# Kernel tuning notes

Measured on AMD Instinct MI355X. Metric: run time of the kernel, lower is better.

Reference implementation:

```python
import jax, jax.numpy as jnp
import numpy as np

V, D, B, NEGS = 100000, 128, 131072, 15
P_DROP = 0.1


def setup_inputs() -> dict:
    key = jax.random.key(0)
    k_t, k_c, k_n, k_m, k_wt = jax.random.split(key, 5)
    target = jax.random.randint(k_t, (B,), 0, V, dtype=jnp.int32)
    context = jax.random.randint(k_c, (B,), 0, V, dtype=jnp.int32)
    # multinomial over uniform noise_dist == uniform randint, with replacement
    neg_idx = jax.random.randint(k_n, (B, NEGS), 0, V, dtype=jnp.int32)
    # inverted dropout mask, p=0.1 (F.dropout default training=True)
    keep = jax.random.uniform(k_m, (B, D)) >= P_DROP
    dropout_mask = keep.astype(jnp.float32) / (1.0 - P_DROP)
    # embeddings_target init: uniform(-0.5/D, 0.5/D); embeddings_context init is zeros
    # in the original, but use small randn so the loss/grads are non-degenerate.
    r = 0.5 / D
    W_target = jax.random.uniform(k_wt, (V, D), minval=-r, maxval=r, dtype=jnp.float32)
    W_context = jax.random.normal(jax.random.fold_in(key, 7), (V, D), dtype=jnp.float32) * r
    return {"target": target, "context": context, "neg_idx": neg_idx,
            "dropout_mask": dropout_mask, "W_target": W_target, "W_context": W_context}


def reference(target, context, neg_idx, dropout_mask, W_target, W_context):
    emb_input = W_target[target] * dropout_mask          # [B, D]
    emb_context = W_context[context]                     # [B, D]
    score = jnp.sum(emb_input * emb_context, axis=1)     # [B]
    pos_loss = jax.nn.log_sigmoid(-score)                # [B]  (matches logsigmoid(-score))
    emb_neg = W_context[neg_idx]                         # [B, NEGS, D]
    neg_score = jnp.einsum('bnd,bd->bn', -emb_neg, emb_input)  # bmm(neg(emb_neg), emb_input)
    noise_loss = jnp.sum(jax.nn.log_sigmoid(neg_score), axis=1)  # [B]
    return -jnp.mean(pos_loss + noise_loss)
```

## Files before the change

kernel.cpp:

```cpp
#include <hip/hip_runtime.h>


#define V_SZ  100000
#define B_TOT 131072
#define DDIM  128
#define NNEG  15
#define NROWS 16
#define SCALE     512.0f
#define INV_SCALE (1.0f / 512.0f)

typedef float floatx2 __attribute__((ext_vector_type(2)));

__device__ __forceinline__ float log_sigmoid_fast(float x) {
    return fminf(x, 0.0f) - __logf(1.0f + __expf(-fabsf(x)));
}

__global__ __launch_bounds__(256) void convert_wc_fp8(
    const float* __restrict__ Wc, uint2* __restrict__ Wc8)
{
    const size_t t = (size_t)blockIdx.x * 256 + threadIdx.x;
    const float4* src = (const float4*)Wc;
    float4 a = src[2 * t];
    float4 b = src[2 * t + 1];
    int lo = 0, hi = 0;
    lo = __builtin_amdgcn_cvt_pk_fp8_f32(a.x * SCALE, a.y * SCALE, lo, false);
    lo = __builtin_amdgcn_cvt_pk_fp8_f32(a.z * SCALE, a.w * SCALE, lo, true);
    hi = __builtin_amdgcn_cvt_pk_fp8_f32(b.x * SCALE, b.y * SCALE, hi, false);
    hi = __builtin_amdgcn_cvt_pk_fp8_f32(b.z * SCALE, b.w * SCALE, hi, true);
    Wc8[t] = make_uint2((unsigned)lo, (unsigned)hi);
}

#define BPB   32
#define NBLK  (B_TOT / BPB)
#define RB    8

__global__ __launch_bounds__(256, 4) void cbow_main_fp8(
    const int* __restrict__ target, const int* __restrict__ context,
    const int* __restrict__ neg_idx, const float* __restrict__ dmask,
    const float* __restrict__ Wt, const unsigned* __restrict__ Wc8,
    float* __restrict__ block_sums)
{
    const int tid  = threadIdx.x;
    const int wave = tid >> 6;
    const int lane = tid & 63;
    const int grp  = lane >> 3;
    const int sub  = lane & 7;
    const int b = blockIdx.x * BPB + wave * 8 + grp;

    const int tgt = target[b];
    const float4* trow = (const float4*)(Wt + (size_t)tgt * DDIM) + 4 * sub;
    const float4* mrow = (const float4*)(dmask + (size_t)b * DDIM) + 4 * sub;
    float e[16];
#pragma unroll
    for (int k = 0; k < 4; ++k) {
        float4 w = trow[k];
        float4 m = mrow[k];
        e[4 * k + 0] = w.x * m.x * INV_SCALE;
        e[4 * k + 1] = w.y * m.y * INV_SCALE;
        e[4 * k + 2] = w.z * m.z * INV_SCALE;
        e[4 * k + 3] = w.w * m.w * INV_SCALE;
    }

    int ridx[NROWS];
    ridx[0] = context[b];
#pragma unroll
    for (int n = 0; n < NNEG; ++n)
        ridx[n + 1] = neg_idx[(size_t)b * NNEG + n];

    float acc = 0.0f;
    for (int rb = 0; rb < NROWS; rb += RB) {
        uint4 c[RB];
#pragma unroll
        for (int j = 0; j < RB; ++j)
            c[j] = ((const uint4*)(Wc8 + (size_t)ridx[rb + j] * (DDIM / 4)))[sub];
#pragma unroll
        for (int j = 0; j < RB; ++j) {
            floatx2 f0 = __builtin_amdgcn_cvt_pk_f32_fp8(c[j].x, false);
            floatx2 f1 = __builtin_amdgcn_cvt_pk_f32_fp8(c[j].x, true);
            floatx2 f2 = __builtin_amdgcn_cvt_pk_f32_fp8(c[j].y, false);
            floatx2 f3 = __builtin_amdgcn_cvt_pk_f32_fp8(c[j].y, true);
            floatx2 f4 = __builtin_amdgcn_cvt_pk_f32_fp8(c[j].z, false);
            floatx2 f5 = __builtin_amdgcn_cvt_pk_f32_fp8(c[j].z, true);
            floatx2 f6 = __builtin_amdgcn_cvt_pk_f32_fp8(c[j].w, false);
            floatx2 f7 = __builtin_amdgcn_cvt_pk_f32_fp8(c[j].w, true);
            float p = f0.x * e[0]  + f0.y * e[1]
                    + f1.x * e[2]  + f1.y * e[3]
                    + f2.x * e[4]  + f2.y * e[5]
                    + f3.x * e[6]  + f3.y * e[7]
                    + f4.x * e[8]  + f4.y * e[9]
                    + f5.x * e[10] + f5.y * e[11]
                    + f6.x * e[12] + f6.y * e[13]
                    + f7.x * e[14] + f7.y * e[15];
            p += __shfl_xor(p, 1);
            p += __shfl_xor(p, 2);
            p += __shfl_xor(p, 4);
            acc += log_sigmoid_fast(-p);
        }
    }

    if (sub != 0) acc = 0.0f;
    acc += __shfl_xor(acc, 8);
    acc += __shfl_xor(acc, 16);
    acc += __shfl_xor(acc, 32);

    __shared__ float wsum[4];
    if (lane == 0) wsum[wave] = acc;
    __syncthreads();
    if (tid == 0)
        block_sums[blockIdx.x] = wsum[0] + wsum[1] + wsum[2] + wsum[3];
}

__global__ __launch_bounds__(256, 4) void cbow_main_f32(
    const int* __restrict__ target, const int* __restrict__ context,
    const int* __restrict__ neg_idx, const float* __restrict__ dmask,
    const float* __restrict__ Wt, const float* __restrict__ Wc,
    float* __restrict__ block_sums)
{
    const int tid  = threadIdx.x;
    const int wave = tid >> 6;
    const int lane = tid & 63;
    const int grp  = lane >> 3;
    const int sub  = lane & 7;
    const int b = blockIdx.x * BPB + wave * 8 + grp;

    const int tgt = target[b];
    const float4* trow = (const float4*)(Wt + (size_t)tgt * DDIM);
    const float4* mrow = (const float4*)(dmask + (size_t)b * DDIM);
    float4 e[4];
#pragma unroll
    for (int k = 0; k < 4; ++k) {
        float4 w = trow[sub + 8 * k];
        float4 m = mrow[sub + 8 * k];
        e[k] = make_float4(w.x * m.x, w.y * m.y, w.z * m.z, w.w * m.w);
    }
    int ridx[NROWS];
    ridx[0] = context[b];
#pragma unroll
    for (int n = 0; n < NNEG; ++n)
        ridx[n + 1] = neg_idx[(size_t)b * NNEG + n];

    float acc = 0.0f;
    for (int rb = 0; rb < NROWS; rb += 4) {
        float4 c[4][4];
#pragma unroll
        for (int j = 0; j < 4; ++j) {
            const float4* crow = (const float4*)(Wc + (size_t)ridx[rb + j] * DDIM);
#pragma unroll
            for (int k = 0; k < 4; ++k) c[j][k] = crow[sub + 8 * k];
        }
#pragma unroll
        for (int j = 0; j < 4; ++j) {
            float p = 0.0f;
#pragma unroll
            for (int k = 0; k < 4; ++k)
                p += c[j][k].x * e[k].x + c[j][k].y * e[k].y
                   + c[j][k].z * e[k].z + c[j][k].w * e[k].w;
            p += __shfl_xor(p, 1);
            p += __shfl_xor(p, 2);
            p += __shfl_xor(p, 4);
            acc += log_sigmoid_fast(-p);
        }
    }
    if (sub != 0) acc = 0.0f;
    acc += __shfl_xor(acc, 8);
    acc += __shfl_xor(acc, 16);
    acc += __shfl_xor(acc, 32);

    __shared__ float wsum[4];
    if (lane == 0) wsum[wave] = acc;
    __syncthreads();
    if (tid == 0)
        block_sums[blockIdx.x] = wsum[0] + wsum[1] + wsum[2] + wsum[3];
}

__global__ __launch_bounds__(256) void cbow_final(
    const float* __restrict__ block_sums, int nblk, float* __restrict__ out)
{
    float s = 0.0f;
    for (int i = threadIdx.x; i < nblk; i += 256) s += block_sums[i];
#pragma unroll
    for (int m = 1; m < 64; m <<= 1) s += __shfl_xor(s, m);
    __shared__ float ws[4];
    if ((threadIdx.x & 63) == 0) ws[threadIdx.x >> 6] = s;
    __syncthreads();
    if (threadIdx.x == 0)
        out[0] = -(ws[0] + ws[1] + ws[2] + ws[3]) / (float)B_TOT;
}

extern "C" void kernel_launch(void* const* d_in, const int* in_sizes, int n_in,
                              void* d_out, int out_size, void* d_ws, size_t ws_size,
                              hipStream_t stream) {
    const int*   target  = (const int*)d_in[0];
    const int*   context = (const int*)d_in[1];
    const int*   neg_idx = (const int*)d_in[2];
    const float* dmask   = (const float*)d_in[3];
    const float* Wt      = (const float*)d_in[4];
    const float* Wc      = (const float*)d_in[5];
    float* out = (float*)d_out;

    float*    block_sums = (float*)d_ws;
    unsigned* Wc8        = (unsigned*)((char*)d_ws + 65536);

    const size_t need = 65536 + (size_t)V_SZ * DDIM;
    if (ws_size >= need) {
        convert_wc_fp8<<<(V_SZ * DDIM / 8 + 255) / 256, 256, 0, stream>>>(
            Wc, (uint2*)Wc8);
        cbow_main_fp8<<<NBLK, 256, 0, stream>>>(target, context, neg_idx,
                                                dmask, Wt, Wc8, block_sums);
    } else {
        cbow_main_f32<<<NBLK, 256, 0, stream>>>(target, context, neg_idx,
                                                dmask, Wt, Wc, block_sums);
    }
    cbow_final<<<1, 256, 0, stream>>>(block_sums, NBLK, out);
}
```

Before: 206.7 us.

## Issue all 16 gathers up front, use packed FMA and DPP reductions

The fp8 main kernel now loads all 16 context and negative rows into registers before any compute, instead of two batches of eight. The goal is more memory-level parallelism for the random gathers. The dot product now uses packed two-wide float multiply-adds on a paired copy of the embedding. The 8-lane reduction uses DPP quad-permute and half-row mirror ops instead of ds_swizzle-style shuffles. The occupancy hint is dropped from launch_bounds, so the higher register use may lower waves per CU.

Result: faster. 201.8 us (-2.3%).

```diff
diff --git a/kernel.cpp b/kernel.cpp
--- a/kernel.cpp
+++ b/kernel.cpp
@@ -13,6 +13,12 @@
 
 __device__ __forceinline__ float log_sigmoid_fast(float x) {
     return fminf(x, 0.0f) - __logf(1.0f + __expf(-fabsf(x)));
+}
+
+template <int CTRL>
+__device__ __forceinline__ float dpp_add(float p) {
+    int r = __builtin_amdgcn_update_dpp(0, __float_as_int(p), CTRL, 0xF, 0xF, true);
+    return p + __int_as_float(r);
 }
 
 __global__ __launch_bounds__(256) void convert_wc_fp8(
@@ -32,9 +38,8 @@
 
 #define BPB   32
 #define NBLK  (B_TOT / BPB)
-#define RB    8
-
-__global__ __launch_bounds__(256, 4) void cbow_main_fp8(
+
+__global__ __launch_bounds__(256) void cbow_main_fp8(
     const int* __restrict__ target, const int* __restrict__ context,
     const int* __restrict__ neg_idx, const float* __restrict__ dmask,
     const float* __restrict__ Wt, const unsigned* __restrict__ Wc8,
@@ -50,15 +55,13 @@
     const int tgt = target[b];
     const float4* trow = (const float4*)(Wt + (size_t)tgt * DDIM) + 4 * sub;
     const float4* mrow = (const float4*)(dmask + (size_t)b * DDIM) + 4 * sub;
-    float e[16];
+    floatx2 e2[8];
 #pragma unroll
     for (int k = 0; k < 4; ++k) {
         float4 w = trow[k];
         float4 m = mrow[k];
-        e[4 * k + 0] = w.x * m.x * INV_SCALE;
-        e[4 * k + 1] = w.y * m.y * INV_SCALE;
-        e[4 * k + 2] = w.z * m.z * INV_SCALE;
-        e[4 * k + 3] = w.w * m.w * INV_SCALE;
+        e2[2 * k + 0] = (floatx2){w.x * m.x * INV_SCALE, w.y * m.y * INV_SCALE};
+        e2[2 * k + 1] = (floatx2){w.z * m.z * INV_SCALE, w.w * m.w * INV_SCALE};
     }
 
     int ridx[NROWS];
@@ -67,35 +70,35 @@
     for (int n = 0; n < NNEG; ++n)
         ridx[n + 1] = neg_idx[(size_t)b * NNEG + n];
 
+    uint4 c[NROWS];
+#pragma unroll
+    for (int r = 0; r < NROWS; ++r)
+        c[r] = ((const uint4*)(Wc8 + (size_t)ridx[r] * (DDIM / 4)))[sub];
+
     float acc = 0.0f;
-    for (int rb = 0; rb < NROWS; rb += RB) {
-        uint4 c[RB];
-#pragma unroll
-        for (int j = 0; j < RB; ++j)
-            c[j] = ((const uint4*)(Wc8 + (size_t)ridx[rb + j] * (DDIM / 4)))[sub];
-#pragma unroll
-        for (int j = 0; j < RB; ++j) {
-            floatx2 f0 = __builtin_amdgcn_cvt_pk_f32_fp8(c[j].x, false);
-            floatx2 f1 = __builtin_amdgcn_cvt_pk_f32_fp8(c[j].x, true);
-            floatx2 f2 = __builtin_amdgcn_cvt_pk_f32_fp8(c[j].y, false);
-            floatx2 f3 = __builtin_amdgcn_cvt_pk_f32_fp8(c[j].y, true);
-            floatx2 f4 = __builtin_amdgcn_cvt_pk_f32_fp8(c[j].z, false);
-            floatx2 f5 = __builtin_amdgcn_cvt_pk_f32_fp8(c[j].z, true);
-            floatx2 f6 = __builtin_amdgcn_cvt_pk_f32_fp8(c[j].w, false);
-            floatx2 f7 = __builtin_amdgcn_cvt_pk_f32_fp8(c[j].w, true);
-            float p = f0.x * e[0]  + f0.y * e[1]
-                    + f1.x * e[2]  + f1.y * e[3]
-                    + f2.x * e[4]  + f2.y * e[5]
-                    + f3.x * e[6]  + f3.y * e[7]
-                    + f4.x * e[8]  + f4.y * e[9]
-                    + f5.x * e[10] + f5.y * e[11]
-                    + f6.x * e[12] + f6.y * e[13]
-                    + f7.x * e[14] + f7.y * e[15];
-            p += __shfl_xor(p, 1);
-            p += __shfl_xor(p, 2);
-            p += __shfl_xor(p, 4);
-            acc += log_sigmoid_fast(-p);
-        }
+#pragma unroll
+    for (int r = 0; r < NROWS; ++r) {
+        floatx2 f0 = __builtin_amdgcn_cvt_pk_f32_fp8(c[r].x, false);
+        floatx2 f1 = __builtin_amdgcn_cvt_pk_f32_fp8(c[r].x, true);
+        floatx2 f2 = __builtin_amdgcn_cvt_pk_f32_fp8(c[r].y, false);
+        floatx2 f3 = __builtin_amdgcn_cvt_pk_f32_fp8(c[r].y, true);
+        floatx2 f4 = __builtin_amdgcn_cvt_pk_f32_fp8(c[r].z, false);
+        floatx2 f5 = __builtin_amdgcn_cvt_pk_f32_fp8(c[r].z, true);
+        floatx2 f6 = __builtin_amdgcn_cvt_pk_f32_fp8(c[r].w, false);
+        floatx2 f7 = __builtin_amdgcn_cvt_pk_f32_fp8(c[r].w, true);
+        floatx2 pa = f0 * e2[0];
+        floatx2 pb = f1 * e2[1];
+        pa += f2 * e2[2];
+        pb += f3 * e2[3];
+        pa += f4 * e2[4];
+        pb += f5 * e2[5];
+        pa += f6 * e2[6];
+        pb += f7 * e2[7];
+        float p = (pa.x + pb.x) + (pa.y + pb.y);
+        p = dpp_add<0xB1>(p);
+        p = dpp_add<0x4E>(p);
+        p = dpp_add<0x141>(p);
+        acc += log_sigmoid_fast(-p);
     }
 
     if (sub != 0) acc = 0.0f;
```
